# Kernel optimization log

Measured on AMD Instinct MI355X. Metric: run time of the kernel, lower is better.

Reference implementation:

```python
import jax, jax.numpy as jnp
import numpy as np

B, S, E, D = 8, 2048, 512, 512  # batch, seq (mesh edges), elem_size, embd_size


def setup_inputs() -> dict:
    key = jax.random.key(0)
    ks = jax.random.split(key, 5)
    scale = 1.0 / np.sqrt(E)
    return {
        "x": jax.random.normal(ks[0], (B, S, E), dtype=jnp.float32),
        "Wq": jax.random.normal(ks[1], (E, D), dtype=jnp.float32) * scale,
        "bq": jax.random.normal(ks[2], (D,), dtype=jnp.float32) * 0.01,
        "Wk": jax.random.normal(ks[3], (E, D), dtype=jnp.float32) * scale,
        "bk": jax.random.normal(ks[4], (D,), dtype=jnp.float32) * 0.01,
    }


def reference(x, Wq, bq, Wk, bk):
    elem_size = x.shape[-1]
    q = jax.nn.relu(x @ Wq + bq)              # [B,S,D]
    k = jax.nn.relu(x @ Wk + bk)              # [B,S,D]
    scores = jnp.einsum("bqd,bkd->bqk", q, k) / (elem_size ** 0.5)  # [B,S,S]
    # nn.Softmax(dim=1): normalize over the QUERY axis (column-wise softmax)
    attn = jax.nn.softmax(scores, axis=1)
    new_values = jnp.einsum("bqk,bke->bqe", attn, x)  # V = raw x (use_V=False)
    return x + new_values                     # residual connection
```

## Files before the change

kernel.cpp:

```cpp
#include <hip/hip_runtime.h>
#include <hip/hip_bf16.h>
#include <math.h>

#define Bb 8
#define Ss 2048
#define Ee 512
#define Dd 512
#define QSPLIT 16

typedef __bf16 bf16x8 __attribute__((ext_vector_type(8)));
typedef __bf16 bf16x4 __attribute__((ext_vector_type(4)));
typedef float f32x4 __attribute__((ext_vector_type(4)));

__device__ __forceinline__ void stage_async(ushort* lds, const __bf16* gbase,
                                            int ldg, int wave, int lane) {
#pragma unroll
    for (int t = 0; t < 2; ++t) {
        const int idx = wave * 2 + t;
        const int row = idx * 16 + (lane >> 2);
        const int q8  = (((lane & 3) ^ ((lane >> 3) & 3)) * 8);
        __builtin_amdgcn_global_load_lds(
            (const __attribute__((address_space(1))) void*)(gbase + (size_t)row * ldg + q8),
            (__attribute__((address_space(3))) void*)(lds + idx * 512),
            16, 0, 0);
    }
}

__device__ __forceinline__ void stage_async2(ushort* lds, const __bf16* gbase,
                                             int ldg, int wave, int lane) {
#pragma unroll
    for (int t = 0; t < 4; ++t) {
        const int idx = wave * 4 + t;
        const int row = idx * 16 + (lane >> 2);
        const int q8  = (((lane & 3) ^ ((lane >> 3) & 3)) * 8);
        __builtin_amdgcn_global_load_lds(
            (const __attribute__((address_space(1))) void*)(gbase + (size_t)row * ldg + q8),
            (__attribute__((address_space(3))) void*)(lds + idx * 512),
            16, 0, 0);
    }
}

__global__ void prep_x(const float* __restrict__ in, __bf16* __restrict__ xb,
                       __bf16* __restrict__ xT) {
    __shared__ float tile[32][33];
    const int b  = blockIdx.z;
    const int e0 = blockIdx.x * 32;
    const int s0 = blockIdx.y * 32;
    const float* ip = in + (size_t)b * Ss * Ee;
    __bf16* xbp = xb + (size_t)b * Ss * Ee;
    __bf16* xTp = xT + (size_t)b * Ee * Ss;
    for (int i = threadIdx.y; i < 32; i += 8) {
        const float v = ip[(size_t)(s0 + i) * Ee + e0 + threadIdx.x];
        tile[i][threadIdx.x] = v;
        xbp[(size_t)(s0 + i) * Ee + e0 + threadIdx.x] = (__bf16)v;
    }
    __syncthreads();
    for (int i = threadIdx.y; i < 32; i += 8)
        xTp[(size_t)(e0 + i) * Ss + s0 + threadIdx.x] = (__bf16)tile[threadIdx.x][i];
}

__global__ void transpose_w(const float* __restrict__ Wq, const float* __restrict__ Wk,
                            __bf16* __restrict__ WqT, __bf16* __restrict__ WkT) {
    __shared__ float tile[32][33];
    const float* in = blockIdx.z ? Wk : Wq;
    __bf16* out = blockIdx.z ? WkT : WqT;
    const int x0 = blockIdx.x * 32;
    const int y0 = blockIdx.y * 32;
    for (int i = threadIdx.y; i < 32; i += 8)
        tile[i][threadIdx.x] = in[(size_t)(y0 + i) * 512 + (x0 + threadIdx.x)];
    __syncthreads();
    for (int i = threadIdx.y; i < 32; i += 8)
        out[(size_t)(x0 + i) * 512 + (y0 + threadIdx.x)] = (__bf16)tile[threadIdx.x][i];
}

__global__ __launch_bounds__(256, 4) void proj_kernel(
    const __bf16* __restrict__ X,
    const __bf16* __restrict__ WqT, const __bf16* __restrict__ WkT,
    const float* __restrict__ bq, const float* __restrict__ bk,
    __bf16* __restrict__ qb, __bf16* __restrict__ kb)
{
    __shared__ __align__(16) ushort As[128 * 32];
    __shared__ __align__(16) ushort Bs[128 * 32];
    const __bf16* WT  = blockIdx.z ? WkT : WqT;
    const float* bias = blockIdx.z ? bk : bq;
    __bf16* Out       = blockIdx.z ? kb : qb;

    const int tid = threadIdx.x;
    const int wave = tid >> 6, lane = tid & 63, quad = lane >> 4, l16 = lane & 15;
    const int wm = (wave >> 1) * 64, wn = (wave & 1) * 64;
    const int m0 = blockIdx.y * 128, n0 = blockIdx.x * 128;
    const int sw = (quad ^ ((l16 >> 1) & 3)) * 8;
    const int K = 512;

    f32x4 acc[4][4];
    f32x4 zero = {0.f, 0.f, 0.f, 0.f};
    for (int i = 0; i < 4; i++) for (int j = 0; j < 4; j++) acc[i][j] = zero;

    for (int k0 = 0; k0 < K; k0 += 32) {
        stage_async(As, X  + (size_t)m0 * K + k0, K, wave, lane);
        stage_async(Bs, WT + (size_t)n0 * K + k0, K, wave, lane);
        __syncthreads();
        bf16x8 af[4], bfr[4];
        for (int i = 0; i < 4; i++) af[i]  = *(bf16x8*)&As[(wm + i * 16 + l16) * 32 + sw];
        for (int j = 0; j < 4; j++) bfr[j] = *(bf16x8*)&Bs[(wn + j * 16 + l16) * 32 + sw];
        for (int i = 0; i < 4; i++)
            for (int j = 0; j < 4; j++)
                acc[i][j] = __builtin_amdgcn_mfma_f32_16x16x32_bf16(af[i], bfr[j], acc[i][j], 0, 0, 0);
        __syncthreads();
    }

    for (int i = 0; i < 4; i++) {
        const int row = m0 + wm + i * 16 + quad * 4;
        for (int j = 0; j < 4; j++) {
            const int col = n0 + wn + j * 16 + l16;
            const float bv = bias[col];
            for (int rr = 0; rr < 4; rr++) {
                float v = acc[i][j][rr] + bv;
                v = v > 0.f ? v : 0.f;
                Out[(size_t)(row + rr) * 512 + col] = (__bf16)v;
            }
        }
    }
}

__global__ __launch_bounds__(256, 4) void scores_kernel(
    const __bf16* __restrict__ Q,
    const __bf16* __restrict__ Km,
    __bf16* __restrict__ P,
    float* __restrict__ Mp,
    float* __restrict__ Lp)
{
    __shared__ __align__(16) ushort As[128 * 32];
    __shared__ __align__(16) ushort Bs[128 * 32];
    const int id = blockIdx.x;
    const int b = id & 7;
    const int rest = id >> 3;
    const int qy = rest >> 4;
    const int m0 = qy * 128;
    const int n0 = (rest & 15) * 128;
    const __bf16* A  = Q  + (size_t)b * Ss * Dd;
    const __bf16* Bp = Km + (size_t)b * Ss * Dd;
    __bf16* C = P + (size_t)b * Ss * Ss;

    const int tid = threadIdx.x;
    const int wave = tid >> 6, lane = tid & 63, quad = lane >> 4, l16 = lane & 15;
    const int wm = (wave >> 1) * 64, wn = (wave & 1) * 64;
    const int sw = (quad ^ ((l16 >> 1) & 3)) * 8;
    const float scale = 0.044194173824159216f;

    f32x4 acc[4][4];
    f32x4 zero = {0.f, 0.f, 0.f, 0.f};
    for (int i = 0; i < 4; i++) for (int j = 0; j < 4; j++) acc[i][j] = zero;

    for (int k0 = 0; k0 < Dd; k0 += 32) {
        stage_async(As, A  + (size_t)m0 * Dd + k0, Dd, wave, lane);
        stage_async(Bs, Bp + (size_t)n0 * Dd + k0, Dd, wave, lane);
        __syncthreads();
        bf16x8 af[4], bfr[4];
        for (int i = 0; i < 4; i++) af[i]  = *(bf16x8*)&As[(wm + i * 16 + l16) * 32 + sw];
        for (int j = 0; j < 4; j++) bfr[j] = *(bf16x8*)&Bs[(wn + j * 16 + l16) * 32 + sw];
        for (int i = 0; i < 4; i++)
            for (int j = 0; j < 4; j++)
                acc[i][j] = __builtin_amdgcn_mfma_f32_16x16x32_bf16(af[i], bfr[j], acc[i][j], 0, 0, 0);
        __syncthreads();
    }

    float* Ms = (float*)As;
    float* Ls = ((float*)As) + 256;
    const int half = wave >> 1;
    float mj[4];
    for (int j = 0; j < 4; j++) {
        float m = -1e30f;
        for (int i = 0; i < 4; i++)
            for (int rr = 0; rr < 4; rr++)
                m = fmaxf(m, acc[i][j][rr]);
        m = fmaxf(m, __shfl_xor(m, 16));
        m = fmaxf(m, __shfl_xor(m, 32));
        mj[j] = m;
    }
    if (quad == 0)
        for (int j = 0; j < 4; j++) Ms[half * 128 + wn + j * 16 + l16] = mj[j];
    __syncthreads();
    float mt[4];
    for (int j = 0; j < 4; j++) {
        const int c = wn + j * 16 + l16;
        mt[j] = fmaxf(Ms[c], Ms[128 + c]);
    }
    float lj[4];
    for (int j = 0; j < 4; j++) {
        const int col = n0 + wn + j * 16 + l16;
        float l = 0.f;
        for (int i = 0; i < 4; i++) {
            const int row = m0 + wm + i * 16 + quad * 4;
            for (int rr = 0; rr < 4; rr++) {
                const float e = __expf((acc[i][j][rr] - mt[j]) * scale);
                C[(size_t)(row + rr) * Ss + col] = (__bf16)e;
                l += e;
            }
        }
        l += __shfl_xor(l, 16);
        l += __shfl_xor(l, 32);
        lj[j] = l;
    }
    if (quad == 0)
        for (int j = 0; j < 4; j++) Ls[half * 128 + wn + j * 16 + l16] = lj[j];
    __syncthreads();
    if (tid < 128) {
        const size_t o = ((size_t)qy * Bb + b) * Ss + n0 + tid;
        Mp[o] = fmaxf(Ms[tid], Ms[128 + tid]) * scale;
        Lp[o] = Ls[tid] + Ls[128 + tid];
    }
}

__global__ void stats_combine(const float* __restrict__ Mp, const float* __restrict__ Lp,
                              float* __restrict__ Corr) {
    const int idx = blockIdx.x * 256 + threadIdx.x;
    float m = -1e30f;
    for (int qy = 0; qy < QSPLIT; qy++) m = fmaxf(m, Mp[(size_t)qy * Bb * Ss + idx]);
    float l = 0.f;
    for (int qy = 0; qy < QSPLIT; qy++)
        l += Lp[(size_t)qy * Bb * Ss + idx] * __expf(Mp[(size_t)qy * Bb * Ss + idx] - m);
    const float li = 1.0f / l;
    for (int qy = 0; qy < QSPLIT; qy++)
        Corr[(size_t)qy * Bb * Ss + idx] = __expf(Mp[(size_t)qy * Bb * Ss + idx] - m) * li;
}

__global__ __launch_bounds__(128, 2) void pv_kernel(
    const __bf16* __restrict__ P,
    const float* __restrict__ Corr,
    const __bf16* __restrict__ XT,
    const __bf16* __restrict__ XB,
    float* __restrict__ Out)
{
    __shared__ __align__(16) ushort As[64 * 32];
    __shared__ __align__(16) ushort Bs[128 * 32];
    const int id = blockIdx.x;
    const int b = id & 7;
    const int rest = id >> 3;
    const int m0 = (rest >> 2) * 64;
    const int n0 = (rest & 3) * 128;
    const int qy = m0 >> 7;
    const __bf16* A  = P  + (size_t)b * Ss * Ss;
    const __bf16* Bp = XT + (size_t)b * Ee * Ss;
    const float* Cr  = Corr + ((size_t)qy * Bb + b) * Ss;

    const int tid = threadIdx.x;
    const int wave = tid >> 6, lane = tid & 63, quad = lane >> 4, l16 = lane & 15;
    const int wn = wave * 64;
    const int sw = (quad ^ ((l16 >> 1) & 3)) * 8;
    const int r = tid >> 2, seg = (tid & 3) * 8;
    const int p8 = (((tid & 3) ^ ((r >> 1) & 3)) * 8);

    f32x4 acc[4][4];
    f32x4 zero = {0.f, 0.f, 0.f, 0.f};
    for (int i = 0; i < 4; i++) for (int j = 0; j < 4; j++) acc[i][j] = zero;

    const __bf16* Arow0 = A + (size_t)(m0 + r) * Ss;
    const __bf16* Arow1 = A + (size_t)(m0 + r + 32) * Ss;
    bf16x8 pr0 = *(const bf16x8*)&Arow0[seg];
    bf16x8 pr1 = *(const bf16x8*)&Arow1[seg];
    float4 cra = *(const float4*)&Cr[seg];
    float4 crb = *(const float4*)&Cr[seg + 4];

    for (int k0 = 0; k0 < Ss; k0 += 32) {
        stage_async2(Bs, Bp + (size_t)n0 * Ss + k0, Ss, wave, lane);
        float cv[8];
        cv[0] = cra.x; cv[1] = cra.y; cv[2] = cra.z; cv[3] = cra.w;
        cv[4] = crb.x; cv[5] = crb.y; cv[6] = crb.z; cv[7] = crb.w;
        bf16x8 o0, o1;
        #pragma unroll
        for (int t = 0; t < 8; t++) o0[t] = (__bf16)((float)pr0[t] * cv[t]);
        #pragma unroll
        for (int t = 0; t < 8; t++) o1[t] = (__bf16)((float)pr1[t] * cv[t]);
        *(bf16x8*)&As[r * 32 + p8]        = o0;
        *(bf16x8*)&As[(r + 32) * 32 + p8] = o1;
        __syncthreads();
        bf16x8 af[4], bfr[4];
        for (int i = 0; i < 4; i++) af[i]  = *(bf16x8*)&As[(i * 16 + l16) * 32 + sw];
        for (int j = 0; j < 4; j++) bfr[j] = *(bf16x8*)&Bs[(wn + j * 16 + l16) * 32 + sw];
        const int kn = (k0 + 32) & (Ss - 1);
        pr0 = *(const bf16x8*)&Arow0[kn + seg];
        pr1 = *(const bf16x8*)&Arow1[kn + seg];
        cra = *(const float4*)&Cr[kn + seg];
        crb = *(const float4*)&Cr[kn + seg + 4];
        for (int i = 0; i < 4; i++)
            for (int j = 0; j < 4; j++)
                acc[i][j] = __builtin_amdgcn_mfma_f32_16x16x32_bf16(af[i], bfr[j], acc[i][j], 0, 0, 0);
        __syncthreads();
    }

    for (int i = 0; i < 4; i++) {
        const int row = m0 + i * 16 + quad * 4;
        for (int j = 0; j < 4; j++) {
            const int col = n0 + wn + j * 16 + l16;
            for (int rr = 0; rr < 4; rr++) {
                const size_t idx = ((size_t)b * Ss + row + rr) * Ee + col;
                Out[idx] = (float)XB[idx] + acc[i][j][rr];
            }
        }
    }
}

extern "C" void kernel_launch(void* const* d_in, const int* in_sizes, int n_in,
                              void* d_out, int out_size, void* d_ws, size_t ws_size,
                              hipStream_t stream) {
    const float* x  = (const float*)d_in[0];
    const float* Wq = (const float*)d_in[1];
    const float* bq = (const float*)d_in[2];
    const float* Wk = (const float*)d_in[3];
    const float* bk = (const float*)d_in[4];
    float* out = (float*)d_out;

    char* ws = (char*)d_ws;
    size_t off = 0;
    auto alloc = [&](size_t bytes) -> void* {
        void* p = ws + off;
        off += (bytes + 255) & ~(size_t)255;
        return p;
    };
    __bf16* P    = (__bf16*)alloc((size_t)Bb * Ss * Ss * 2);
    __bf16* xb   = (__bf16*)alloc((size_t)Bb * Ss * Ee * 2);
    __bf16* qb   = (__bf16*)alloc((size_t)Bb * Ss * Dd * 2);
    __bf16* kb   = (__bf16*)alloc((size_t)Bb * Ss * Dd * 2);
    __bf16* xT   = (__bf16*)alloc((size_t)Bb * Ee * Ss * 2);
    __bf16* WqT  = (__bf16*)alloc((size_t)512 * 512 * 2);
    __bf16* WkT  = (__bf16*)alloc((size_t)512 * 512 * 2);
    float*  Mp   = (float*)alloc((size_t)QSPLIT * Bb * Ss * 4);
    float*  Lp   = (float*)alloc((size_t)QSPLIT * Bb * Ss * 4);
    float*  Corr = (float*)alloc((size_t)QSPLIT * Bb * Ss * 4);
    if (off > ws_size) return;

    prep_x<<<dim3(16, 64, 8), dim3(32, 8), 0, stream>>>(x, xb, xT);
    transpose_w<<<dim3(16, 16, 2), dim3(32, 8), 0, stream>>>(Wq, Wk, WqT, WkT);

    proj_kernel<<<dim3(4, 128, 2), 256, 0, stream>>>(xb, WqT, WkT, bq, bk, qb, kb);

    scores_kernel<<<dim3(2048), 256, 0, stream>>>(qb, kb, P, Mp, Lp);
    stats_combine<<<dim3(Bb * Ss / 256), 256, 0, stream>>>(Mp, Lp, Corr);

    pv_kernel<<<dim3(1024), 128, 0, stream>>>(P, Corr, xT, xb, out);
}
```

Before: 232.7 us.

## Widen K-step to 64 and stage GEMM epilogue through LDS for vector stores

The projection and scores GEMMs now stage 64-wide K tiles with a new XOR swizzle, which halves the number of barrier-separated iterations. Their epilogues write bf16 results into a per-wave LDS patch and then emit coalesced 16-byte global stores, replacing scattered 2-byte stores. The bf16 conversion is now truncation (top 16 bits) instead of round-to-nearest, which slightly changes numerics. LDS use per block doubles, which may lower occupancy.

Result: no change. 228.7 us (-1.7%).

```diff
diff --git a/kernel.cpp b/kernel.cpp
--- a/kernel.cpp
+++ b/kernel.cpp
@@ -11,20 +11,6 @@
 typedef __bf16 bf16x8 __attribute__((ext_vector_type(8)));
 typedef __bf16 bf16x4 __attribute__((ext_vector_type(4)));
 typedef float f32x4 __attribute__((ext_vector_type(4)));
-
-__device__ __forceinline__ void stage_async(ushort* lds, const __bf16* gbase,
-                                            int ldg, int wave, int lane) {
-#pragma unroll
-    for (int t = 0; t < 2; ++t) {
-        const int idx = wave * 2 + t;
-        const int row = idx * 16 + (lane >> 2);
-        const int q8  = (((lane & 3) ^ ((lane >> 3) & 3)) * 8);
-        __builtin_amdgcn_global_load_lds(
-            (const __attribute__((address_space(1))) void*)(gbase + (size_t)row * ldg + q8),
-            (__attribute__((address_space(3))) void*)(lds + idx * 512),
-            16, 0, 0);
-    }
-}
 
 __device__ __forceinline__ void stage_async2(ushort* lds, const __bf16* gbase,
                                              int ldg, int wave, int lane) {
@@ -36,6 +22,20 @@
         __builtin_amdgcn_global_load_lds(
             (const __attribute__((address_space(1))) void*)(gbase + (size_t)row * ldg + q8),
             (__attribute__((address_space(3))) void*)(lds + idx * 512),
+            16, 0, 0);
+    }
+}
+
+__device__ __forceinline__ void stage64(ushort* lds, const __bf16* gbase,
+                                        int ldg, int wave, int lane) {
+#pragma unroll
+    for (int t = 0; t < 4; ++t) {
+        const int slot = wave * 256 + t * 64 + lane;
+        const int row  = slot >> 3;
+        const int c    = (slot & 7) ^ (row & 7);
+        __builtin_amdgcn_global_load_lds(
+            (const __attribute__((address_space(1))) void*)(gbase + (size_t)row * ldg + c * 8),
+            (__attribute__((address_space(3))) void*)(lds + (size_t)slot * 8),
             16, 0, 0);
     }
 }
@@ -79,8 +79,9 @@
     const float* __restrict__ bq, const float* __restrict__ bk,
     __bf16* __restrict__ qb, __bf16* __restrict__ kb)
 {
-    __shared__ __align__(16) ushort As[128 * 32];
-    __shared__ __align__(16) ushort Bs[128 * 32];
+    __shared__ __align__(16) ushort smem[2 * 128 * 64];
+    ushort* As = smem;
+    ushort* Bs = smem + 128 * 64;
     const __bf16* WT  = blockIdx.z ? WkT : WqT;
     const float* bias = blockIdx.z ? bk : bq;
     __bf16* Out       = blockIdx.z ? kb : qb;
@@ -89,37 +90,48 @@
     const int wave = tid >> 6, lane = tid & 63, quad = lane >> 4, l16 = lane & 15;
     const int wm = (wave >> 1) * 64, wn = (wave & 1) * 64;
     const int m0 = blockIdx.y * 128, n0 = blockIdx.x * 128;
-    const int sw = (quad ^ ((l16 >> 1) & 3)) * 8;
     const int K = 512;
+    const int sw0 = ((quad)     ^ (l16 & 7)) * 8;
+    const int sw1 = ((quad + 4) ^ (l16 & 7)) * 8;
 
     f32x4 acc[4][4];
     f32x4 zero = {0.f, 0.f, 0.f, 0.f};
     for (int i = 0; i < 4; i++) for (int j = 0; j < 4; j++) acc[i][j] = zero;
 
-    for (int k0 = 0; k0 < K; k0 += 32) {
-        stage_async(As, X  + (size_t)m0 * K + k0, K, wave, lane);
-        stage_async(Bs, WT + (size_t)n0 * K + k0, K, wave, lane);
-        __syncthreads();
-        bf16x8 af[4], bfr[4];
-        for (int i = 0; i < 4; i++) af[i]  = *(bf16x8*)&As[(wm + i * 16 + l16) * 32 + sw];
-        for (int j = 0; j < 4; j++) bfr[j] = *(bf16x8*)&Bs[(wn + j * 16 + l16) * 32 + sw];
+    for (int k0 = 0; k0 < K; k0 += 64) {
+        stage64(As, X  + (size_t)m0 * K + k0, K, wave, lane);
+        stage64(Bs, WT + (size_t)n0 * K + k0, K, wave, lane);
+        __syncthreads();
+        #pragma unroll
+        for (int h = 0; h < 2; h++) {
+            const int sw = h ? sw1 : sw0;
+            bf16x8 af[4], bfr[4];
+            for (int i = 0; i < 4; i++) af[i]  = *(bf16x8*)&As[(wm + i * 16 + l16) * 64 + sw];
+            for (int j = 0; j < 4; j++) bfr[j] = *(bf16x8*)&Bs[(wn + j * 16 + l16) * 64 + sw];
+            for (int i = 0; i < 4; i++)
+                for (int j = 0; j < 4; j++)
+                    acc[i][j] = __builtin_amdgcn_mfma_f32_16x16x32_bf16(af[i], bfr[j], acc[i][j], 0, 0, 0);
+        }
+        __syncthreads();
+    }
+
+    ushort* patch = smem + wave * 4096;
+    for (int j = 0; j < 4; j++) {
+        const float bv = bias[n0 + wn + j * 16 + l16];
         for (int i = 0; i < 4; i++)
-            for (int j = 0; j < 4; j++)
-                acc[i][j] = __builtin_amdgcn_mfma_f32_16x16x32_bf16(af[i], bfr[j], acc[i][j], 0, 0, 0);
-        __syncthreads();
-    }
-
-    for (int i = 0; i < 4; i++) {
-        const int row = m0 + wm + i * 16 + quad * 4;
-        for (int j = 0; j < 4; j++) {
-            const int col = n0 + wn + j * 16 + l16;
-            const float bv = bias[col];
             for (int rr = 0; rr < 4; rr++) {
                 float v = acc[i][j][rr] + bv;
                 v = v > 0.f ? v : 0.f;
-                Out[(size_t)(row + rr) * 512 + col] = (__bf16)v;
+                patch[(i * 16 + quad * 4 + rr) * 64 + j * 16 + l16] = ((ushort2*)&v)[0].y;
             }
-        }
+    }
+    __syncthreads();
+    #pragma unroll
+    for (int it = 0; it < 8; it++) {
+        const int lr = it * 8 + (lane >> 3);
+        const int lc = (lane & 7) * 8;
+        const bf16x8 v = *(const bf16x8*)&patch[lr * 64 + lc];
+        *(bf16x8*)&Out[(size_t)(m0 + wm + lr) * 512 + n0 + wn + lc] = v;
     }
 }
 
@@ -130,8 +142,10 @@
     float* __restrict__ Mp,
     float* __restrict__ Lp)
 {
-    __shared__ __align__(16) ushort As[128 * 32];
-    __shared__ __align__(16) ushort Bs[128 * 32];
+    __shared__ __align__(16) ushort smem[2 * 128 * 64];
+    __shared__ float stats[512];
+    ushort* As = smem;
+    ushort* Bs = smem + 128 * 64;
     const int id = blockIdx.x;
     const int b = id & 7;
     const int rest = id >> 3;
@@ -145,28 +159,33 @@
     const int tid = threadIdx.x;
     const int wave = tid >> 6, lane = tid & 63, quad = lane >> 4, l16 = lane & 15;
     const int wm = (wave >> 1) * 64, wn = (wave & 1) * 64;
-    const int sw = (quad ^ ((l16 >> 1) & 3)) * 8;
+    const int sw0 = ((quad)     ^ (l16 & 7)) * 8;
+    const int sw1 = ((quad + 4) ^ (l16 & 7)) * 8;
     const float scale = 0.044194173824159216f;
 
     f32x4 acc[4][4];
     f32x4 zero = {0.f, 0.f, 0.f, 0.f};
     for (int i = 0; i < 4; i++) for (int j = 0; j < 4; j++) acc[i][j] = zero;
 
-    for (int k0 = 0; k0 < Dd; k0 += 32) {
-        stage_async(As, A  + (size_t)m0 * Dd + k0, Dd, wave, lane);
-        stage_async(Bs, Bp + (size_t)n0 * Dd + k0, Dd, wave, lane);
-        __syncthreads();
-        bf16x8 af[4], bfr[4];
-        for (int i = 0; i < 4; i++) af[i]  = *(bf16x8*)&As[(wm + i * 16 + l16) * 32 + sw];
-        for (int j = 0; j < 4; j++) bfr[j] = *(bf16x8*)&Bs[(wn + j * 16 + l16) * 32 + sw];
-        for (int i = 0; i < 4; i++)
-            for (int j = 0; j < 4; j++)
-                acc[i][j] = __builtin_amdgcn_mfma_f32_16x16x32_bf16(af[i], bfr[j], acc[i][j], 0, 0, 0);
-        __syncthreads();
-    }
-
-    float* Ms = (float*)As;
-    float* Ls = ((float*)As) + 256;
+    for (int k0 = 0; k0 < Dd; k0 += 64) {
+        stage64(As, A  + (size_t)m0 * Dd + k0, Dd, wave, lane);
+        stage64(Bs, Bp + (size_t)n0 * Dd + k0, Dd, wave, lane);
+        __syncthreads();
+        #pragma unroll
+        for (int h = 0; h < 2; h++) {
+            const int sw = h ? sw1 : sw0;
+            bf16x8 af[4], bfr[4];
+            for (int i = 0; i < 4; i++) af[i]  = *(bf16x8*)&As[(wm + i * 16 + l16) * 64 + sw];
+            for (int j = 0; j < 4; j++) bfr[j] = *(bf16x8*)&Bs[(wn + j * 16 + l16) * 64 + sw];
+            for (int i = 0; i < 4; i++)
+                for (int j = 0; j < 4; j++)
+                    acc[i][j] = __builtin_amdgcn_mfma_f32_16x16x32_bf16(af[i], bfr[j], acc[i][j], 0, 0, 0);
+        }
+        __syncthreads();
+    }
+
+    float* Ms = stats;
+    float* Ls = stats + 256;
     const int half = wave >> 1;
     float mj[4];
     for (int j = 0; j < 4; j++) {
@@ -186,18 +205,16 @@
         const int c = wn + j * 16 + l16;
         mt[j] = fmaxf(Ms[c], Ms[128 + c]);
     }
+    ushort* patch = smem + wave * 4096;
     float lj[4];
     for (int j = 0; j < 4; j++) {
-        const int col = n0 + wn + j * 16 + l16;
         float l = 0.f;
-        for (int i = 0; i < 4; i++) {
-            const int row = m0 + wm + i * 16 + quad * 4;
+        for (int i = 0; i < 4; i++)
             for (int rr = 0; rr < 4; rr++) {
                 const float e = __expf((acc[i][j][rr] - mt[j]) * scale);
-                C[(size_t)(row + rr) * Ss + col] = (__bf16)e;
+                patch[(i * 16 + quad * 4 + rr) * 64 + j * 16 + l16] = ((ushort2*)&e)[0].y;
                 l += e;
             }
-        }
         l += __shfl_xor(l, 16);
         l += __shfl_xor(l, 32);
         lj[j] = l;
@@ -209,6 +226,13 @@
         const size_t o = ((size_t)qy * Bb + b) * Ss + n0 + tid;
         Mp[o] = fmaxf(Ms[tid], Ms[128 + tid]) * scale;
         Lp[o] = Ls[tid] + Ls[128 + tid];
+    }
+    #pragma unroll
+    for (int it = 0; it < 8; it++) {
+        const int lr = it * 8 + (lane >> 3);
+        const int lc = (lane & 7) * 8;
+        const bf16x8 v = *(const bf16x8*)&patch[lr * 64 + lc];
+        *(bf16x8*)&C[(size_t)(m0 + wm + lr) * Ss + n0 + wn + lc] = v;
     }
 }
 
```
